# Kernel optimization log

Measured on AMD Instinct MI355X. Metric: run time of the kernel, lower is better.

The kernel has to match this reference:

```python
import jax, jax.numpy as jnp
from jax import lax
import numpy as np

B, S, N, F, H = 8, 64, 256, 16, 16
C = N * H  # temporal conv channels = 4096
ALPHA = 0.2
EPS = 1e-5
NEG = -9e15


def setup_inputs() -> dict:
    key = jax.random.key(0)
    ks = jax.random.split(key, 10)
    x = jax.random.normal(ks[0], (B, S, N, F), dtype=jnp.float32)
    adj = jax.random.normal(ks[1], (N, N), dtype=jnp.float32)
    W = jax.random.normal(ks[2], (F, H), dtype=jnp.float32) * (1.414 / np.sqrt(F))
    a = jax.random.normal(ks[3], (2 * H,), dtype=jnp.float32) * (1.414 / np.sqrt(2 * H))
    a1, a2 = a[:H], a[H:]
    conv_w = jax.random.normal(ks[4], (C, C, 3), dtype=jnp.float32) * (1.0 / np.sqrt(C * 3))
    conv_b = jnp.zeros((C,), dtype=jnp.float32)
    bn_gamma = jnp.ones((C,), dtype=jnp.float32)
    bn_beta = jnp.zeros((C,), dtype=jnp.float32)
    bn_mean = jnp.zeros((C,), dtype=jnp.float32)
    bn_var = jnp.ones((C,), dtype=jnp.float32)
    ln_gamma = jnp.ones((H,), dtype=jnp.float32)
    ln_beta = jnp.zeros((H,), dtype=jnp.float32)
    return {"x": x, "adj": adj, "W": W, "a1": a1, "a2": a2,
            "conv_w": conv_w, "conv_b": conv_b,
            "bn_gamma": bn_gamma, "bn_beta": bn_beta,
            "bn_mean": bn_mean, "bn_var": bn_var,
            "ln_gamma": ln_gamma, "ln_beta": ln_beta}


def reference(x, adj, W, a1, a2, conv_w, conv_b, bn_gamma, bn_beta, bn_mean, bn_var, ln_gamma, ln_beta):
    b, s, n, f = x.shape
    h = W.shape[1]
    # --- GAT, batched over all timesteps (eval mode: dropout is identity) ---
    Wh = jnp.einsum('bsnf,fh->bsnh', x, W)            # (B,S,N,H)
    # e_ij = LeakyReLU(a1.Wh_i + a2.Wh_j), equivalent to concat-then-matmul
    f1 = jnp.einsum('bsnh,h->bsn', Wh, a1)
    f2 = jnp.einsum('bsnh,h->bsn', Wh, a2)
    e = jax.nn.leaky_relu(f1[..., :, None] + f2[..., None, :], ALPHA)  # (B,S,N,N)
    e = jnp.where(adj > 0, e, NEG)
    attn = jax.nn.softmax(e, axis=-1)
    spatial = jnp.einsum('bsij,bsjh->bsih', attn, Wh)  # (B,S,N,H)
    # --- temporal conv over seq dim, channels = N*H ---
    t = spatial.reshape(b, s, n * h).transpose(0, 2, 1)  # (B,C,S)
    y = lax.conv_general_dilated(t, conv_w, window_strides=(1,), padding=[(1, 1)],
                                 dimension_numbers=('NCH', 'OIH', 'NCH'))
    y = y + conv_b[None, :, None]
    # BatchNorm1d in eval mode
    y = (y - bn_mean[None, :, None]) / jnp.sqrt(bn_var + EPS)[None, :, None]
    y = y * bn_gamma[None, :, None] + bn_beta[None, :, None]
    y = jax.nn.relu(y)
    temp = y.transpose(0, 2, 1).reshape(b, s, n, h)
    # residual is identity since in_features == hidden_dim
    out = temp + x
    # LayerNorm over last dim
    mu = out.mean(-1, keepdims=True)
    var = out.var(-1, keepdims=True)
    out = (out - mu) / jnp.sqrt(var + EPS) * ln_gamma + ln_beta
    return out
```

## Files before the change

kernel.cpp:

```cpp
#include <hip/hip_runtime.h>
#include <stdint.h>

#define ALPHA 0.2f
#define EPSV  1e-5f

typedef unsigned short u16;
typedef unsigned int   u32;
typedef unsigned long long u64;
typedef __bf16 bf16x8 __attribute__((ext_vector_type(8)));
typedef __bf16 bf16x2 __attribute__((ext_vector_type(2)));
typedef float  f32x4  __attribute__((ext_vector_type(4)));

#define NB 8
#define NS 64
#define NN 256
#define NF 16
#define NH 16
#define NC 4096
#define NK 12288
#define NP 512
#define SROW 66
#define BKT 32

__device__ __forceinline__ u16 f2b(float f){
  u32 u = __float_as_uint(f);
  u32 r = u + 0x7fffu + ((u>>16)&1u);
  return (u16)(r>>16);
}
__device__ __forceinline__ void un2(u32 v, float& lo, float& hi){
  lo = __uint_as_float(v<<16); hi = __uint_as_float(v & 0xffff0000u);
}
__device__ __forceinline__ void gld16(void* lds, const void* g){
  __builtin_amdgcn_global_load_lds((const __attribute__((address_space(1))) u32*)g,
                                   (__attribute__((address_space(3))) u32*)lds, 16, 0, 0);
}
__device__ __forceinline__ uint4 cvt8(f32x4 a, f32x4 b){
  union { uint4 u; bf16x2 h[4]; } r;
  r.h[0] = (bf16x2){(__bf16)a[0], (__bf16)a[1]};
  r.h[1] = (bf16x2){(__bf16)a[2], (__bf16)a[3]};
  r.h[2] = (bf16x2){(__bf16)b[0], (__bf16)b[1]};
  r.h[3] = (bf16x2){(__bf16)b[2], (__bf16)b[3]};
  return r.u;
}
__device__ __forceinline__ uint2 cvt4(float a, float b, float c, float d){
  union { uint2 u; bf16x2 h[2]; } r;
  r.h[0] = (bf16x2){(__bf16)a, (__bf16)b};
  r.h[1] = (bf16x2){(__bf16)c, (__bf16)d};
  return r.u;
}

__global__ __launch_bounds__(256) void k_adj(const float* __restrict__ adj,
                                             u64* __restrict__ am,
                                             uint4* __restrict__ spz){
  int w = threadIdx.x>>6, l = threadIdx.x&63;
  int row = blockIdx.x*4 + w;
  #pragma unroll
  for(int g=0;g<4;g++){
    float v = adj[(size_t)row*NN + g*64 + l];
    u64 m = __ballot(v > 0.f);
    if(l==0) am[row*4+g] = m;
  }
  if(spz){
    int g = blockIdx.x*256 + threadIdx.x;
    if(g < 8192){
      int r = g>>9;
      int b = r>>1;
      size_t prow = (size_t)b*SROW + ((r&1) ? (SROW-1) : 0);
      spz[prow*512 + (g&511)] = (uint4){0,0,0,0};
    }
  }
}

__global__ __launch_bounds__(256) void k_cw(const float* __restrict__ cw,
                                            u16* __restrict__ Bw){
  int t = threadIdx.x, co = blockIdx.x;
  const float* src = cw + (size_t)co*NK;
  u16* dst = Bw + (size_t)co*NK;
  #pragma unroll
  for(int i=0;i<4;i++){
    int ci0 = (i*256 + t)*4;
    const f32x4* p = (const f32x4*)(src + (size_t)ci0*3);
    f32x4 v0 = p[0];
    f32x4 v1 = p[1];
    f32x4 v2 = p[2];
    uint2 q0 = cvt4(v0[0], v0[3], v1[2], v2[1]);
    uint2 q1 = cvt4(v0[1], v1[0], v1[3], v2[2]);
    uint2 q2 = cvt4(v0[2], v1[1], v2[0], v2[3]);
    *(uint2*)(dst + 0*NC + ci0) = q0;
    *(uint2*)(dst + 1*NC + ci0) = q1;
    *(uint2*)(dst + 2*NC + ci0) = q2;
  }
}

__global__ __launch_bounds__(256) void k_attn(
    const float* __restrict__ x, const float* __restrict__ W,
    const float* __restrict__ a1, const float* __restrict__ a2,
    const u64* __restrict__ am, u16* __restrict__ Sp){
  __shared__ __align__(16) float Ws[NF][NH];
  __shared__ float a1s[NH], a2s[NH];
  __shared__ __align__(16) float Whs[NN][NH];
  __shared__ float f2s[NN];
  int t = threadIdx.x, bs = blockIdx.x;
  int b = bs>>6, s = bs&63;
  Ws[t>>4][t&15] = W[t];
  if(t<NH){ a1s[t]=a1[t]; a2s[t]=a2[t]; }
  u64 mg[4];
  #pragma unroll
  for(int g=0;g<4;g++) mg[g] = am[t*4+g];
  __syncthreads();

  const float* xp = x + ((size_t)bs*NN + t)*NF;
  float xr[16];
  #pragma unroll
  for(int g=0;g<4;g++) *(f32x4*)&xr[g*4] = ((const f32x4*)xp)[g];
  float wh[16];
  #pragma unroll
  for(int h=0;h<16;h++) wh[h]=0.f;
  #pragma unroll
  for(int f=0;f<16;f++){
    float xf = xr[f];
    #pragma unroll
    for(int h=0;h<16;h++) wh[h] = fmaf(xf, Ws[f][h], wh[h]);
  }
  float fi=0.f, s2=0.f;
  #pragma unroll
  for(int h=0;h<16;h++){ fi=fmaf(wh[h],a1s[h],fi); s2=fmaf(wh[h],a2s[h],s2); }
  #pragma unroll
  for(int g=0;g<4;g++) ((f32x4*)Whs[t])[g] = *(f32x4*)&wh[g*4];
  f2s[t] = s2;
  __syncthreads();

  float den = 0.f;
  f32x4 a0={0,0,0,0}, a1v={0,0,0,0}, a2v={0,0,0,0}, a3v={0,0,0,0};
  #pragma unroll
  for(int g=0;g<4;g++){
    u64 mm = mg[g];
    for(int jj=0;jj<64;jj++){
      int j = g*64+jj;
      float e = fi + f2s[j];
      e = e > 0.f ? e : ALPHA*e;
      float p = ((mm>>jj)&1ull) ? __expf(e) : 0.f;
      den += p;
      const f32x4* wr = (const f32x4*)Whs[j];
      a0 += wr[0]*p; a1v += wr[1]*p; a2v += wr[2]*p; a3v += wr[3]*p;
    }
  }
  float inv = 1.f/fmaxf(den, 1e-30f);
  f32x4 o0 = a0*inv, o1 = a1v*inv, o2 = a2v*inv, o3 = a3v*inv;

  uint4 w0 = cvt8(o0,o1), w1 = cvt8(o2,o3);
  uint4* op = (uint4*)(Sp + ((size_t)(b*SROW + s + 1))*NC) + t*2;
  op[0] = w0; op[1] = w1;
}

__global__ __launch_bounds__(512, 2) void k_gemm(
    const u16* __restrict__ Asp, const u16* __restrict__ Bw,
    u16* __restrict__ yp, int kchunk){
  __shared__ __align__(16) u16 As[4][256*BKT];
  __shared__ __align__(16) u16 Bs[4][256*BKT];
  int t = threadIdx.x;

  int mI, nI, part;
  if(gridDim.y == 8){
    int lin = blockIdx.y*32 + blockIdx.x;
    int xcd = lin & 7, u = lin >> 3;
    nI = xcd*2 + (u&1); mI = (u>>1)&1; part = u>>2;
  } else {
    mI = blockIdx.x & 1; nI = blockIdx.x >> 1; part = blockIdx.y;
  }
  int m0 = mI*256, n0 = nI*256;
  int kbeg = part*kchunk;
  int NT = kchunk / BKT;

  int c0 = t, c1 = 512 + t;
  int rA0 = c0>>2, rA1 = c1>>2;
  int g0 = (c0&3) ^ ((rA0>>1)&3);
  int g1 = (c1&3) ^ ((rA1>>1)&3);
  int mr0 = m0 + rA0, mr1 = m0 + rA1;
  const u16* gaA0 = Asp + (size_t)((mr0>>6)*SROW + (mr0&63))*NC + kbeg + g0*8;
  const u16* gaA1 = Asp + (size_t)((mr1>>6)*SROW + (mr1&63))*NC + kbeg + g1*8;
  const u16* gbB0 = Bw  + (size_t)(n0 + rA0)*NK + kbeg + g0*8;
  const u16* gbB1 = Bw  + (size_t)(n0 + rA1)*NK + kbeg + g1*8;
  int dA0 = c0*8, dA1 = c1*8;

  int l = t & 63, w = t >> 6;
  int wr = w >> 2, wc = w & 3;
  int q = l >> 4, r16 = l & 15;

  int offA[8], offB[4];
  #pragma unroll
  for(int mt=0;mt<8;mt++){
    int row = wr*128 + mt*16 + r16;
    offA[mt] = row*BKT + ((q ^ ((row>>1)&3))*8);
  }
  #pragma unroll
  for(int nt=0;nt<4;nt++){
    int row = wc*64 + nt*16 + r16;
    offB[nt] = row*BKT + ((q ^ ((row>>1)&3))*8);
  }

  f32x4 acc[8][4];
  #pragma unroll
  for(int i=0;i<8;i++)
    #pragma unroll
    for(int j=0;j<4;j++) acc[i][j] = (f32x4){0,0,0,0};

  #pragma unroll
  for(int Tt=0; Tt<3; ++Tt){
    size_t ko = (size_t)Tt*BKT;
    gld16(&As[Tt][dA0], gaA0 + ko); gld16(&As[Tt][dA1], gaA1 + ko);
    gld16(&Bs[Tt][dA0], gbB0 + ko); gld16(&Bs[Tt][dA1], gbB1 + ko);
  }

  #define COMPUTE(BUF)                                                        \
  {                                                                           \
    const u16* ab = As[(BUF)];                                                \
    const u16* bb_ = Bs[(BUF)];                                               \
    bf16x8 af[8], bfr[4];                                                     \
    _Pragma("unroll")                                                         \
    for(int mt=0;mt<8;mt++) af[mt] = *(const bf16x8*)(ab + offA[mt]);         \
    _Pragma("unroll")                                                         \
    for(int nt=0;nt<4;nt++) bfr[nt] = *(const bf16x8*)(bb_ + offB[nt]);       \
    __builtin_amdgcn_s_setprio(1);                                            \
    _Pragma("unroll")                                                         \
    for(int mt=0;mt<8;mt++)                                                   \
      _Pragma("unroll")                                                       \
      for(int nt=0;nt<4;nt++)                                                 \
        acc[mt][nt] = __builtin_amdgcn_mfma_f32_16x16x32_bf16(                \
            af[mt], bfr[nt], acc[mt][nt], 0,0,0);                             \
    __builtin_amdgcn_s_setprio(0);                                            \
  }

  for(int T=0; T<NT-2; ++T){
    __builtin_amdgcn_sched_barrier(0);
    asm volatile("s_waitcnt vmcnt(8)" ::: "memory");
    __builtin_amdgcn_s_barrier();
    __builtin_amdgcn_sched_barrier(0);
    if(T+3 < NT){
      int b3 = (T+3)&3;
      size_t ko = (size_t)(T+3)*BKT;
      gld16(&As[b3][dA0], gaA0 + ko); gld16(&As[b3][dA1], gaA1 + ko);
      gld16(&Bs[b3][dA0], gbB0 + ko); gld16(&Bs[b3][dA1], gbB1 + ko);
    }
    COMPUTE(T&3);
  }
  __builtin_amdgcn_sched_barrier(0);
  asm volatile("s_waitcnt vmcnt(4)" ::: "memory");
  __builtin_amdgcn_s_barrier();
  __builtin_amdgcn_sched_barrier(0);
  COMPUTE((NT-2)&3);
  __builtin_amdgcn_sched_barrier(0);
  asm volatile("s_waitcnt vmcnt(0)" ::: "memory");
  __builtin_amdgcn_s_barrier();
  __builtin_amdgcn_sched_barrier(0);
  COMPUTE((NT-1)&3);
  #undef COMPUTE

  u16* op = yp + (size_t)part*NP*NC;
  #pragma unroll
  for(int mt=0;mt<8;mt++)
    #pragma unroll
    for(int nt=0;nt<4;nt++)
      #pragma unroll
      for(int rr=0;rr<4;rr++){
        int m = m0 + wr*128 + mt*16 + q*4 + rr;
        int n = n0 + wc*64 + nt*16 + r16;
        op[(size_t)m*NC + n] = f2b(acc[mt][nt][rr]);
      }
}

__global__ __launch_bounds__(256) void k_attn_s(
    const float* __restrict__ x, const float* __restrict__ W,
    const float* __restrict__ a1, const float* __restrict__ a2,
    const u64* __restrict__ am, u16* __restrict__ Bt){
  __shared__ __align__(16) float Ws[NF][NH];
  __shared__ float a1s[NH], a2s[NH];
  __shared__ __align__(16) float Whs[NN][NH];
  __shared__ float f2s[NN];
  int t = threadIdx.x, bs = blockIdx.x;
  int b = bs>>6, s = bs&63;
  Ws[t>>4][t&15] = W[t];
  if(t<NH){ a1s[t]=a1[t]; a2s[t]=a2[t]; }
  u64 mg[4];
  #pragma unroll
  for(int g=0;g<4;g++) mg[g] = am[t*4+g];
  __syncthreads();

  const float* xp = x + ((size_t)bs*NN + t)*NF;
  float xr[16];
  #pragma unroll
  for(int g=0;g<4;g++) *(f32x4*)&xr[g*4] = ((const f32x4*)xp)[g];
  float wh[16];
  #pragma unroll
  for(int h=0;h<16;h++) wh[h]=0.f;
  #pragma unroll
  for(int f=0;f<16;f++){
    float xf = xr[f];
    #pragma unroll
    for(int h=0;h<16;h++) wh[h] = fmaf(xf, Ws[f][h], wh[h]);
  }
  float fi=0.f, s2=0.f;
  #pragma unroll
  for(int h=0;h<16;h++){ fi=fmaf(wh[h],a1s[h],fi); s2=fmaf(wh[h],a2s[h],s2); }
  #pragma unroll
  for(int g=0;g<4;g++) ((f32x4*)Whs[t])[g] = *(f32x4*)&wh[g*4];
  f2s[t] = s2;
  __syncthreads();

  float den = 0.f;
  f32x4 a0={0,0,0,0}, a1v={0,0,0,0}, a2v={0,0,0,0}, a3v={0,0,0,0};
  #pragma unroll
  for(int g=0;g<4;g++){
    u64 mm = mg[g];
    for(int jj=0;jj<64;jj++){
      int j = g*64+jj;
      float e = fi + f2s[j];
      e = e > 0.f ? e : ALPHA*e;
      float p = ((mm>>jj)&1ull) ? __expf(e) : 0.f;
      den += p;
      const f32x4* wr = (const f32x4*)Whs[j];
      a0 += wr[0]*p; a1v += wr[1]*p; a2v += wr[2]*p; a3v += wr[3]*p;
    }
  }
  float inv = 1.f/fmaxf(den, 1e-30f);
  float vals[16];
  *(f32x4*)&vals[0]  = a0*inv;  *(f32x4*)&vals[4]  = a1v*inv;
  *(f32x4*)&vals[8]  = a2v*inv; *(f32x4*)&vals[12] = a3v*inv;

  #pragma unroll
  for(int k=0;k<3;k++){
    int cs = s + 1 - k;
    if(cs >= 0 && cs < NS){
      size_t base = ((size_t)(b*NS+cs))*NK + (size_t)t*48 + k;
      #pragma unroll
      for(int h=0;h<16;h++) Bt[base + h*3] = f2b(vals[h]);
    }
  }
  if(s == 0){
    size_t base = ((size_t)(b*NS))*NK + (size_t)t*48;
    #pragma unroll
    for(int h=0;h<16;h++) Bt[base + h*3] = 0;
  }
  if(s == NS-1){
    size_t base = ((size_t)(b*NS+NS-1))*NK + (size_t)t*48 + 2;
    #pragma unroll
    for(int h=0;h<16;h++) Bt[base + h*3] = 0;
  }
}

__global__ __launch_bounds__(256) void k_gemm_f(
    const u16* __restrict__ Abt, const float* __restrict__ Bwf,
    u16* __restrict__ yp, int kchunk){
  __shared__ __align__(16) u16 As0[128*32];
  __shared__ __align__(16) u16 As1[128*32];
  __shared__ __align__(16) u16 Bs0[128*32];
  __shared__ __align__(16) u16 Bs1[128*32];
  int t = threadIdx.x;
  int id = blockIdx.x;
  int xr_ = id & 7, q0 = id >> 3;
  int mI = q0 & 3, nhi = q0 >> 2;
  int m0 = mI*128, n0 = (nhi*8 + xr_)*128;
  int kbeg = blockIdx.y*kchunk;
  f32x4 acc[4][4];
  #pragma unroll
  for(int i=0;i<4;i++)
    #pragma unroll
    for(int j=0;j<4;j++) acc[i][j] = (f32x4){0,0,0,0};

  int l = t&63, w = t>>6;
  int wm = (w&1)*64, wn = (w>>1)*64;
  int q = l>>4, r16 = l&15;

  int c0 = t, c1 = t+256;
  const u16*   ga0 = Abt + (size_t)(m0 + (c0>>2))*NK + (c0&3)*8;
  const u16*   ga1 = Abt + (size_t)(m0 + (c1>>2))*NK + (c1&3)*8;
  const float* gb0 = Bwf + (size_t)(n0 + (c0>>2))*NK + (c0&3)*8;
  const float* gb1 = Bwf + (size_t)(n0 + (c1>>2))*NK + (c1&3)*8;
  u16 *la00 = As0 + c0*8, *la01 = As0 + c1*8;
  u16 *la10 = As1 + c0*8, *la11 = As1 + c1*8;
  u16 *lb00 = Bs0 + c0*8, *lb01 = Bs0 + c1*8;
  u16 *lb10 = Bs1 + c0*8, *lb11 = Bs1 + c1*8;

  for(int kk=0; kk<kchunk; kk+=64){
    int k0 = kbeg + kk;
    f32x4 v00a = *(const f32x4*)(gb0 + k0);
    f32x4 v00b = *(const f32x4*)(gb0 + k0 + 4);
    f32x4 v01a = *(const f32x4*)(gb1 + k0);
    f32x4 v01b = *(const f32x4*)(gb1 + k0 + 4);
    f32x4 v10a = *(const f32x4*)(gb0 + k0 + 32);
    f32x4 v10b = *(const f32x4*)(gb0 + k0 + 36);
    f32x4 v11a = *(const f32x4*)(gb1 + k0 + 32);
    f32x4 v11b = *(const f32x4*)(gb1 + k0 + 36);
    uint4 w00 = cvt8(v00a, v00b);
    uint4 w01 = cvt8(v01a, v01b);
    uint4 w10 = cvt8(v10a, v10b);
    uint4 w11 = cvt8(v11a, v11b);
    __syncthreads();
    gld16(la00, ga0 + k0);      gld16(la01, ga1 + k0);
    gld16(la10, ga0 + k0 + 32); gld16(la11, ga1 + k0 + 32);
    *(uint4*)lb00 = w00; *(uint4*)lb01 = w01;
    *(uint4*)lb10 = w10; *(uint4*)lb11 = w11;
    __syncthreads();
    {
      bf16x8 af[4], bfr[4];
      #pragma unroll
      for(int mt=0;mt<4;mt++) af[mt]  = *(const bf16x8*)(As0 + (wm+mt*16+r16)*32 + q*8);
      #pragma unroll
      for(int nt=0;nt<4;nt++) bfr[nt] = *(const bf16x8*)(Bs0 + (wn+nt*16+r16)*32 + q*8);
      #pragma unroll
      for(int mt=0;mt<4;mt++)
        #pragma unroll
        for(int nt=0;nt<4;nt++)
          acc[mt][nt] = __builtin_amdgcn_mfma_f32_16x16x32_bf16(af[mt], bfr[nt], acc[mt][nt], 0,0,0);
    }
    {
      bf16x8 af[4], bfr[4];
      #pragma unroll
      for(int mt=0;mt<4;mt++) af[mt]  = *(const bf16x8*)(As1 + (wm+mt*16+r16)*32 + q*8);
      #pragma unroll
      for(int nt=0;nt<4;nt++) bfr[nt] = *(const bf16x8*)(Bs1 + (wn+nt*16+r16)*32 + q*8);
      #pragma unroll
      for(int mt=0;mt<4;mt++)
        #pragma unroll
        for(int nt=0;nt<4;nt++)
          acc[mt][nt] = __builtin_amdgcn_mfma_f32_16x16x32_bf16(af[mt], bfr[nt], acc[mt][nt], 0,0,0);
    }
  }
  u16* op = yp + (size_t)blockIdx.y*NP*NC;
  #pragma unroll
  for(int mt=0;mt<4;mt++)
    #pragma unroll
    for(int nt=0;nt<4;nt++)
      #pragma unroll
      for(int rr=0;rr<4;rr++){
        int m = m0 + wm + mt*16 + q*4 + rr;
        int n = n0 + wn + nt*16 + r16;
        op[(size_t)m*NC + n] = f2b(acc[mt][nt][rr]);
      }
}

__global__ __launch_bounds__(256) void k_post(
    const u16* __restrict__ yp, int nparts,
    const float* __restrict__ x,
    const float* __restrict__ cb, const float* __restrict__ bg,
    const float* __restrict__ bb, const float* __restrict__ bm,
    const float* __restrict__ bv, const float* __restrict__ lg,
    const float* __restrict__ lb, float* __restrict__ out){
  int n = threadIdx.x, bs = blockIdx.x;
  float v[16];
  #pragma unroll
  for(int h=0;h<16;h++) v[h]=0.f;
  for(int p=0;p<nparts;p++){
    const u16* pp = yp + (size_t)p*NP*NC + (size_t)bs*NC + n*16;
    uint4 u0 = ((const uint4*)pp)[0];
    uint4 u1 = ((const uint4*)pp)[1];
    float lo, hi;
    un2(u0.x,lo,hi); v[0]+=lo;  v[1]+=hi;
    un2(u0.y,lo,hi); v[2]+=lo;  v[3]+=hi;
    un2(u0.z,lo,hi); v[4]+=lo;  v[5]+=hi;
    un2(u0.w,lo,hi); v[6]+=lo;  v[7]+=hi;
    un2(u1.x,lo,hi); v[8]+=lo;  v[9]+=hi;
    un2(u1.y,lo,hi); v[10]+=lo; v[11]+=hi;
    un2(u1.z,lo,hi); v[12]+=lo; v[13]+=hi;
    un2(u1.w,lo,hi); v[14]+=lo; v[15]+=hi;
  }
  const float* xp = x + ((size_t)bs*NN + n)*NH;
  float xr[16];
  #pragma unroll
  for(int g=0;g<4;g++) *(f32x4*)&xr[g*4] = ((const f32x4*)xp)[g];

  float mu = 0.f;
  #pragma unroll
  for(int h=0;h<16;h++){
    int co = n*16 + h;
    float t1 = v[h] + cb[co];
    t1 = (t1 - bm[co]) * (1.f/sqrtf(bv[co] + EPSV));
    t1 = t1 * bg[co] + bb[co];
    t1 = fmaxf(t1, 0.f);
    t1 += xr[h];
    v[h] = t1; mu += t1;
  }
  mu *= (1.f/16.f);
  float var = 0.f;
  #pragma unroll
  for(int h=0;h<16;h++){ float d = v[h]-mu; var = fmaf(d,d,var); }
  var *= (1.f/16.f);
  float rs = 1.f/sqrtf(var + EPSV);
  float* op = out + ((size_t)bs*NN + n)*NH;
  #pragma unroll
  for(int h=0;h<16;h++) op[h] = (v[h]-mu)*rs*lg[h] + lb[h];
}

extern "C" void kernel_launch(void* const* d_in, const int* in_sizes, int n_in,
                              void* d_out, int out_size, void* d_ws, size_t ws_size,
                              hipStream_t stream){
  const float* x   = (const float*)d_in[0];
  const float* adj = (const float*)d_in[1];
  const float* W   = (const float*)d_in[2];
  const float* a1  = (const float*)d_in[3];
  const float* a2  = (const float*)d_in[4];
  const float* cw  = (const float*)d_in[5];
  const float* cb  = (const float*)d_in[6];
  const float* bg  = (const float*)d_in[7];
  const float* bb  = (const float*)d_in[8];
  const float* bm  = (const float*)d_in[9];
  const float* bv  = (const float*)d_in[10];
  const float* lg  = (const float*)d_in[11];
  const float* lb  = (const float*)d_in[12];
  float* out = (float*)d_out;

  char* ws = (char*)d_ws;
  const size_t ypb = (size_t)NP*NC*2;

  const size_t SP_OFF  = 8192;
  const size_t SP_SZ   = (size_t)NB*SROW*NC*2;
  const size_t BW_OFF  = SP_OFF + SP_SZ;
  const size_t BW_SZ   = (size_t)NC*NK*2;
  const size_t YP_OFF2 = BW_OFF + BW_SZ;

  u64* am = (u64*)ws;

  int P2 = 0;
  if(ws_size >= YP_OFF2 + 8*ypb)      P2 = 8;
  else if(ws_size >= YP_OFF2 + 4*ypb) P2 = 4;
  else if(ws_size >= YP_OFF2 + 2*ypb) P2 = 2;
  else if(ws_size >= YP_OFF2 + 1*ypb) P2 = 1;

  if(P2){
    u16* Sp = (u16*)(ws + SP_OFF);
    u16* Bw = (u16*)(ws + BW_OFF);
    u16* yp = (u16*)(ws + YP_OFF2);
    hipLaunchKernelGGL(k_adj,  dim3(64),      dim3(256), 0, stream, adj, am, (uint4*)Sp);
    hipLaunchKernelGGL(k_cw,   dim3(NC),      dim3(256), 0, stream, cw, Bw);
    hipLaunchKernelGGL(k_attn, dim3(NP),      dim3(256), 0, stream, x,W,a1,a2,am,Sp);
    hipLaunchKernelGGL(k_gemm, dim3(32,P2),   dim3(512), 0, stream, Sp, Bw, yp, NK/P2);
    hipLaunchKernelGGL(k_post, dim3(NP),      dim3(256), 0, stream, yp,P2,x,cb,bg,bb,bm,bv,lg,lb,out);
  } else {
    const size_t BT_OFF = 8192;
    const size_t YP_OFF = BT_OFF + (size_t)NP*NK*2;
    int P = 1;
    if(ws_size >= YP_OFF + 8*ypb)      P = 8;
    else if(ws_size >= YP_OFF + 4*ypb) P = 4;
    else if(ws_size >= YP_OFF + 2*ypb) P = 2;
    u16* Bt = (u16*)(ws + BT_OFF);
    u16* yp = (u16*)(ws + YP_OFF);
    hipLaunchKernelGGL(k_adj,    dim3(64),     dim3(256), 0, stream, adj, am, (uint4*)0);
    hipLaunchKernelGGL(k_attn_s, dim3(NP),     dim3(256), 0, stream, x,W,a1,a2,am,Bt);
    hipLaunchKernelGGL(k_gemm_f, dim3(128,P),  dim3(256), 0, stream, Bt, cw, yp, NK/P);
    hipLaunchKernelGGL(k_post,   dim3(NP),     dim3(256), 0, stream, yp,P,x,cb,bg,bb,bm,bv,lg,lb,out);
  }
}
```

Before: 444.2 us.

## Fuse conv weight fp32-to-bf16 conversion into GEMM, add im2col activation pass

```diff
diff --git a/kernel.cpp b/kernel.cpp
--- a/kernel.cpp
+++ b/kernel.cpp
@@ -42,12 +42,6 @@
   r.h[3] = (bf16x2){(__bf16)b[2], (__bf16)b[3]};
   return r.u;
 }
-__device__ __forceinline__ uint2 cvt4(float a, float b, float c, float d){
-  union { uint2 u; bf16x2 h[2]; } r;
-  r.h[0] = (bf16x2){(__bf16)a, (__bf16)b};
-  r.h[1] = (bf16x2){(__bf16)c, (__bf16)d};
-  return r.u;
-}
 
 __global__ __launch_bounds__(256) void k_adj(const float* __restrict__ adj,
                                              u64* __restrict__ am,
@@ -68,27 +62,6 @@
       size_t prow = (size_t)b*SROW + ((r&1) ? (SROW-1) : 0);
       spz[prow*512 + (g&511)] = (uint4){0,0,0,0};
     }
-  }
-}
-
-__global__ __launch_bounds__(256) void k_cw(const float* __restrict__ cw,
-                                            u16* __restrict__ Bw){
-  int t = threadIdx.x, co = blockIdx.x;
-  const float* src = cw + (size_t)co*NK;
-  u16* dst = Bw + (size_t)co*NK;
-  #pragma unroll
-  for(int i=0;i<4;i++){
-    int ci0 = (i*256 + t)*4;
-    const f32x4* p = (const f32x4*)(src + (size_t)ci0*3);
-    f32x4 v0 = p[0];
-    f32x4 v1 = p[1];
-    f32x4 v2 = p[2];
-    uint2 q0 = cvt4(v0[0], v0[3], v1[2], v2[1]);
-    uint2 q1 = cvt4(v0[1], v1[0], v1[3], v2[2]);
-    uint2 q2 = cvt4(v0[2], v1[1], v2[0], v2[3]);
-    *(uint2*)(dst + 0*NC + ci0) = q0;
-    *(uint2*)(dst + 1*NC + ci0) = q1;
-    *(uint2*)(dst + 2*NC + ci0) = q2;
   }
 }
 
@@ -153,11 +126,32 @@
   op[0] = w0; op[1] = w1;
 }
 
+__global__ __launch_bounds__(256) void k_i2c(const u16* __restrict__ Sp,
+                                             u16* __restrict__ Bt){
+  int t = threadIdx.x, col = blockIdx.x;
+  int b = col>>6, s = col&63;
+  const u16* r0 = Sp + ((size_t)(b*SROW + s))*NC + t*16;
+  union { uint4 q[2]; u16 h[16]; } a0, a1, a2;
+  a0.q[0]=((const uint4*)r0)[0];        a0.q[1]=((const uint4*)r0)[1];
+  a1.q[0]=((const uint4*)(r0+NC))[0];   a1.q[1]=((const uint4*)(r0+NC))[1];
+  a2.q[0]=((const uint4*)(r0+2*NC))[0]; a2.q[1]=((const uint4*)(r0+2*NC))[1];
+  union { uint4 q[6]; u16 h[48]; } o;
+  #pragma unroll
+  for(int i=0;i<16;i++){
+    o.h[3*i]   = a0.h[i];
+    o.h[3*i+1] = a1.h[i];
+    o.h[3*i+2] = a2.h[i];
+  }
+  uint4* dst = (uint4*)(Bt + (size_t)col*NK + t*48);
+  #pragma unroll
+  for(int j=0;j<6;j++) dst[j] = o.q[j];
+}
+
 __global__ __launch_bounds__(512, 2) void k_gemm(
-    const u16* __restrict__ Asp, const u16* __restrict__ Bw,
+    const u16* __restrict__ Abt, const float* __restrict__ Bwf,
     u16* __restrict__ yp, int kchunk){
-  __shared__ __align__(16) u16 As[4][256*BKT];
-  __shared__ __align__(16) u16 Bs[4][256*BKT];
+  __shared__ __align__(16) u16 As[3][256*BKT];
+  __shared__ __align__(16) u16 Bs[3][256*BKT];
   int t = threadIdx.x;
 
   int mI, nI, part;
@@ -176,12 +170,15 @@
   int rA0 = c0>>2, rA1 = c1>>2;
   int g0 = (c0&3) ^ ((rA0>>1)&3);
   int g1 = (c1&3) ^ ((rA1>>1)&3);
-  int mr0 = m0 + rA0, mr1 = m0 + rA1;
-  const u16* gaA0 = Asp + (size_t)((mr0>>6)*SROW + (mr0&63))*NC + kbeg + g0*8;
-  const u16* gaA1 = Asp + (size_t)((mr1>>6)*SROW + (mr1&63))*NC + kbeg + g1*8;
-  const u16* gbB0 = Bw  + (size_t)(n0 + rA0)*NK + kbeg + g0*8;
-  const u16* gbB1 = Bw  + (size_t)(n0 + rA1)*NK + kbeg + g1*8;
+  const u16* gaA0 = Abt + (size_t)(m0 + rA0)*NK + kbeg + g0*8;
+  const u16* gaA1 = Abt + (size_t)(m0 + rA1)*NK + kbeg + g1*8;
   int dA0 = c0*8, dA1 = c1*8;
+
+  int rowB = t>>1, halfB = t&1;
+  const float* gbB = Bwf + (size_t)(n0 + rowB)*NK + kbeg + halfB*16;
+  int gB0 = (halfB*2 + 0) ^ ((rowB>>1)&3);
+  int gB1 = (halfB*2 + 1) ^ ((rowB>>1)&3);
+  int dB0 = rowB*BKT + gB0*8, dB1 = rowB*BKT + gB1*8;
 
   int l = t & 63, w = t >> 6;
   int wr = w >> 2, wc = w & 3;
@@ -205,16 +202,19 @@
     #pragma unroll
     for(int j=0;j<4;j++) acc[i][j] = (f32x4){0,0,0,0};
 
-  #pragma unroll
-  for(int Tt=0; Tt<3; ++Tt){
-    size_t ko = (size_t)Tt*BKT;
-    gld16(&As[Tt][dA0], gaA0 + ko); gld16(&As[Tt][dA1], gaA1 + ko);
-    gld16(&Bs[Tt][dA0], gbB0 + ko); gld16(&Bs[Tt][dA1], gbB1 + ko);
-  }
-
+  f32x4 rb0[4], rb1[4];
+
+  #define ISSUE_A(TT) { size_t ko=(size_t)(TT)*BKT; int bf=(TT)%3;            \
+    gld16(&As[bf][dA0], gaA0+ko); gld16(&As[bf][dA1], gaA1+ko); }
+  #define LOAD_B(TT, R) { size_t ko=(size_t)(TT)*BKT;                         \
+    R[0]=*(const f32x4*)(gbB+ko);    R[1]=*(const f32x4*)(gbB+ko+4);          \
+    R[2]=*(const f32x4*)(gbB+ko+8);  R[3]=*(const f32x4*)(gbB+ko+12); }
+  #define DSW_B(TT, R) { int bf=(TT)%3;                                       \
+    uint4 w0_=cvt8(R[0],R[1]), w1_=cvt8(R[2],R[3]);                           \
+    *(uint4*)&Bs[bf][dB0] = w0_; *(uint4*)&Bs[bf][dB1] = w1_; }
   #define COMPUTE(BUF)                                                        \
   {                                                                           \
-    const u16* ab = As[(BUF)];                                                \
+    const u16* ab  = As[(BUF)];                                               \
     const u16* bb_ = Bs[(BUF)];                                               \
     bf16x8 af[8], bfr[4];                                                     \
     _Pragma("unroll")                                                         \
@@ -231,30 +231,38 @@
     __builtin_amdgcn_s_setprio(0);                                            \
   }
 
-  for(int T=0; T<NT-2; ++T){
-    __builtin_amdgcn_sched_barrier(0);
-    asm volatile("s_waitcnt vmcnt(8)" ::: "memory");
-    __builtin_amdgcn_s_barrier();
-    __builtin_amdgcn_sched_barrier(0);
-    if(T+3 < NT){
-      int b3 = (T+3)&3;
-      size_t ko = (size_t)(T+3)*BKT;
-      gld16(&As[b3][dA0], gaA0 + ko); gld16(&As[b3][dA1], gaA1 + ko);
-      gld16(&Bs[b3][dA0], gbB0 + ko); gld16(&Bs[b3][dA1], gbB1 + ko);
-    }
-    COMPUTE(T&3);
-  }
+  ISSUE_A(0);
+  LOAD_B(0, rb0);
+  asm volatile("s_waitcnt vmcnt(0)" ::: "memory");
   __builtin_amdgcn_sched_barrier(0);
-  asm volatile("s_waitcnt vmcnt(4)" ::: "memory");
+  DSW_B(0, rb0);
+  LOAD_B(1, rb0);
+  ISSUE_A(1);
+  asm volatile("s_waitcnt lgkmcnt(0)" ::: "memory");
   __builtin_amdgcn_s_barrier();
   __builtin_amdgcn_sched_barrier(0);
-  COMPUTE((NT-2)&3);
-  __builtin_amdgcn_sched_barrier(0);
-  asm volatile("s_waitcnt vmcnt(0)" ::: "memory");
-  __builtin_amdgcn_s_barrier();
-  __builtin_amdgcn_sched_barrier(0);
-  COMPUTE((NT-1)&3);
+
+  #define GITER(T, RCUR, RNXT) {                                              \
+    if((T) < NT-1){ asm volatile("s_waitcnt vmcnt(2)" ::: "memory"); }        \
+    else          { asm volatile("s_waitcnt vmcnt(0)" ::: "memory"); }        \
+    __builtin_amdgcn_sched_barrier(0);                                        \
+    if((T) < NT-1){ DSW_B((T)+1, RCUR); }                                     \
+    asm volatile("s_waitcnt lgkmcnt(0)" ::: "memory");                        \
+    __builtin_amdgcn_s_barrier();                                             \
+    __builtin_amdgcn_sched_barrier(0);                                        \
+    if((T)+2 < NT){ LOAD_B((T)+2, RNXT); ISSUE_A((T)+2); }                    \
+    COMPUTE((T)%3);                                                           \
+  }
+
+  for(int T=0; T<NT; T+=2){
+    GITER(T,   rb0, rb1);
+    GITER(T+1, rb1, rb0);
+  }
+  #undef GITER
   #undef COMPUTE
+  #undef DSW_B
+  #undef LOAD_B
+  #undef ISSUE_A
 
   u16* op = yp + (size_t)part*NP*NC;
   #pragma unroll
@@ -514,9 +522,9 @@
 
   const size_t SP_OFF  = 8192;
   const size_t SP_SZ   = (size_t)NB*SROW*NC*2;
-  const size_t BW_OFF  = SP_OFF + SP_SZ;
-  const size_t BW_SZ   = (size_t)NC*NK*2;
-  const size_t YP_OFF2 = BW_OFF + BW_SZ;
+  const size_t BT_OFF2 = SP_OFF + SP_SZ;
+  const size_t BT_SZ   = (size_t)NP*NK*2;
+  const size_t YP_OFF2 = BT_OFF2 + BT_SZ;
 
   u64* am = (u64*)ws;
 
@@ -528,12 +536,12 @@
 
   if(P2){
     u16* Sp = (u16*)(ws + SP_OFF);
-    u16* Bw = (u16*)(ws + BW_OFF);
+    u16* Bt = (u16*)(ws + BT_OFF2);
     u16* yp = (u16*)(ws + YP_OFF2);
     hipLaunchKernelGGL(k_adj,  dim3(64),      dim3(256), 0, stream, adj, am, (uint4*)Sp);
-    hipLaunchKernelGGL(k_cw,   dim3(NC),      dim3(256), 0, stream, cw, Bw);
     hipLaunchKernelGGL(k_attn, dim3(NP),      dim3(256), 0, stream, x,W,a1,a2,am,Sp);
-    hipLaunchKernelGGL(k_gemm, dim3(32,P2),   dim3(512), 0, stream, Sp, Bw, yp, NK/P2);
+    hipLaunchKernelGGL(k_i2c,  dim3(NP),      dim3(256), 0, stream, Sp, Bt);
+    hipLaunchKernelGGL(k_gemm, dim3(32,P2),   dim3(512), 0, stream, Bt, cw, yp, NK/P2);
     hipLaunchKernelGGL(k_post, dim3(NP),      dim3(256), 0, stream, yp,P2,x,cb,bg,bb,bm,bv,lg,lb,out);
   } else {
     const size_t BT_OFF = 8192;
```

Result: faster. 416.7 us (-6.2%).
